# Optimization experiments

Measured on AMD Instinct MI355X. Metric: run time of the kernel, lower is better.

Reference implementation:

```python
import jax, jax.numpy as jnp
import numpy as np

B, C, H, W, N = 2, 64, 512, 512, 150000


def setup_inputs() -> dict:
    key = jax.random.key(0)
    k = jax.random.split(key, 6)
    return {
        "before_pseudoimages": jax.random.normal(k[0], (B, C, H, W), jnp.float32),
        "after_pseudoimages": jax.random.normal(k[1], (B, C, H, W), jnp.float32),
        "point_offsets": jax.random.normal(k[2], (B, N, 3), jnp.float32),
        "voxel_coords": jax.random.randint(k[3], (B, N, 3), 0, 512, jnp.int32),
        "W1": jax.random.normal(k[4], (131, 32), jnp.float32) * 0.08,
        "b1": jnp.zeros((32,), jnp.float32),
        "W2": jax.random.normal(k[5], (32, 3), jnp.float32) * 0.18,
        "b2": jnp.zeros((3,), jnp.float32),
    }


def reference(before_pseudoimages, after_pseudoimages, point_offsets, voxel_coords,
              W1, b1, W2, b2):
    # voxel_coords[..., 0] is the Z index, asserted == 0 in the original; unused.
    ys = voxel_coords[..., 1]  # [B, N]
    xs = voxel_coords[..., 2]  # [B, N]

    def gather(img, y, x):
        # img: [C, H, W] -> gathered [N, C]  (matches pseudoimage[:, y, x].T)
        return img[:, y, x].T

    before_vecs = jax.vmap(gather)(before_pseudoimages, ys, xs)  # [B, N, C]
    after_vecs = jax.vmap(gather)(after_pseudoimages, ys, xs)    # [B, N, C]
    feats = jnp.concatenate([before_vecs, after_vecs, point_offsets], axis=-1)  # [B, N, 131]

    h = jax.nn.gelu(jnp.einsum("bnf,fh->bnh", feats, W1) + b1, approximate=False)
    flow = jnp.einsum("bnh,ho->bno", h, W2) + b2  # [B, N, 3]
    return flow
```

## Files before the change

### kernel.cpp

```cpp
#include <hip/hip_runtime.h>
#include <math.h>

#define NCH   64
#define IMW   512
#define NPTS  150000
#define TOTAL (2 * NPTS)
#define IMHW  (512 * 512)
#define HID   32
#define NBINS 32768


__global__ __launch_bounds__(256) void hist_kernel(const int* __restrict__ coords,
                                                   int* __restrict__ hist) {
    int gid = blockIdx.x * blockDim.x + threadIdx.x;
    if (gid >= TOTAL) return;
    const int y = coords[gid * 3 + 1];
    const int x = coords[gid * 3 + 2];
    const int b = (gid >= NPTS) ? 1 : 0;
    const int key = (b << 14) | (y << 5) | (x >> 4);
    atomicAdd(&hist[key], 1);
}

__global__ __launch_bounds__(1024) void scan_kernel(const int* __restrict__ hist,
                                                    int* __restrict__ binPos) {
    __shared__ int lds[1024];
    const int t = threadIdx.x;
    const int base = t * 32;
    int loc[32];
    int s = 0;
    #pragma unroll
    for (int i = 0; i < 32; ++i) { loc[i] = s; s += hist[base + i]; }
    lds[t] = s;
    __syncthreads();
    for (int d = 1; d < 1024; d <<= 1) {
        int v = lds[t];
        int add = (t >= d) ? lds[t - d] : 0;
        __syncthreads();
        lds[t] = v + add;
        __syncthreads();
    }
    const int excl = lds[t] - s;
    #pragma unroll
    for (int i = 0; i < 32; ++i) binPos[base + i] = excl + loc[i];
}

__global__ __launch_bounds__(256) void scatter_kernel(const int* __restrict__ coords,
                                                      int* __restrict__ binPos,
                                                      int* __restrict__ perm) {
    int gid = blockIdx.x * blockDim.x + threadIdx.x;
    if (gid >= TOTAL) return;
    const int y = coords[gid * 3 + 1];
    const int x = coords[gid * 3 + 2];
    const int b = (gid >= NPTS) ? 1 : 0;
    const int key = (b << 14) | (y << 5) | (x >> 4);
    const int pos = atomicAdd(&binPos[key], 1);
    perm[pos] = gid;
}


#define LOADCH(buf, cbase)                                             \
    _Pragma("unroll")                                                  \
    for (int j = 0; j < 16; ++j) buf[j] = img_ptr[(long)((cbase) + j) * IMHW];

#define FMACH(buf, cbase)                                              \
    _Pragma("unroll")                                                  \
    for (int j = 0; j < 16; ++j) {                                     \
        const float* wr = w1b + ((cbase) + j) * HID;                   \
        _Pragma("unroll")                                              \
        for (int h = 0; h < HID; ++h) acc[h] = fmaf(buf[j], wr[h], acc[h]); \
    }

__global__ __launch_bounds__(256) void ffd_kernel(
    const float* __restrict__ before,
    const float* __restrict__ after,
    const float* __restrict__ offsets,
    const int*   __restrict__ coords,
    const float* __restrict__ W1,
    const float* __restrict__ b1,
    const float* __restrict__ W2,
    const float* __restrict__ b2,
    const int*   __restrict__ perm,
    float*       __restrict__ out)
{
    __shared__ float xch[HID][128];

    const int lp  = threadIdx.x & 127;
    const int img = __builtin_amdgcn_readfirstlane(threadIdx.x >> 7);
    const int gpt = blockIdx.x * 128 + lp;
    const bool valid = gpt < TOTAL;

    int pid = 0;
    if (valid) pid = perm ? perm[gpt] : gpt;

    const long pbase = (long)pid * 3;
    int y = 0, x = 0;
    if (valid) { y = coords[pbase + 1]; x = coords[pbase + 2]; }
    const int b = (pid >= NPTS) ? 1 : 0;

    const float* img_ptr = (img ? after : before) +
                           (long)b * NCH * IMHW + (long)y * IMW + x;
    const float* w1b = W1 + img * 64 * HID;

    float acc[HID];
    if (img == 0) {
        float o0 = 0.f, o1 = 0.f, o2 = 0.f;
        if (valid) { o0 = offsets[pbase]; o1 = offsets[pbase + 1]; o2 = offsets[pbase + 2]; }
        const float* r0 = W1 + 128 * HID;
        const float* r1 = W1 + 129 * HID;
        const float* r2 = W1 + 130 * HID;
        #pragma unroll
        for (int h = 0; h < HID; ++h)
            acc[h] = fmaf(o2, r2[h], fmaf(o1, r1[h], fmaf(o0, r0[h], b1[h])));
    } else {
        #pragma unroll
        for (int h = 0; h < HID; ++h) acc[h] = 0.f;
    }

    if (valid) {
        float g0[16], g1[16];
        LOADCH(g0, 0)
        LOADCH(g1, 16)
        FMACH(g0, 0)
        LOADCH(g0, 32)
        FMACH(g1, 16)
        LOADCH(g1, 48)
        FMACH(g0, 32)
        FMACH(g1, 48)
    }

    if (img == 1) {
        #pragma unroll
        for (int h = 0; h < HID; ++h) xch[h][lp] = acc[h];
    }
    __syncthreads();
    if (img == 0 && valid) {
        #pragma unroll
        for (int h = 0; h < HID; ++h) acc[h] += xch[h][lp];

        #pragma unroll
        for (int h = 0; h < HID; ++h) {
            const float xh = acc[h];
            acc[h] = 0.5f * xh * (1.0f + erff(xh * 0.70710678118654752f));
        }

        float o0 = b2[0], o1 = b2[1], o2 = b2[2];
        #pragma unroll
        for (int h = 0; h < HID; ++h) {
            o0 = fmaf(acc[h], W2[h * 3 + 0], o0);
            o1 = fmaf(acc[h], W2[h * 3 + 1], o1);
            o2 = fmaf(acc[h], W2[h * 3 + 2], o2);
        }
        out[pbase + 0] = o0;
        out[pbase + 1] = o1;
        out[pbase + 2] = o2;
    }
}

extern "C" void kernel_launch(void* const* d_in, const int* in_sizes, int n_in,
                              void* d_out, int out_size, void* d_ws, size_t ws_size,
                              hipStream_t stream) {
    const float* before  = (const float*)d_in[0];
    const float* after   = (const float*)d_in[1];
    const float* offsets = (const float*)d_in[2];
    const int*   coords  = (const int*)  d_in[3];
    const float* W1      = (const float*)d_in[4];
    const float* b1      = (const float*)d_in[5];
    const float* W2      = (const float*)d_in[6];
    const float* b2      = (const float*)d_in[7];
    float* out = (float*)d_out;

    const int block = 256;
    const int sgrid = (TOTAL + block - 1) / block;
    const int fgrid = (TOTAL + 127) / 128;

    const size_t need = (size_t)(2 * NBINS + TOTAL) * sizeof(int);

    if (ws_size >= need) {
        int* hist   = (int*)d_ws;
        int* binPos = hist + NBINS;
        int* perm   = binPos + NBINS;

        hipMemsetAsync(hist, 0, NBINS * sizeof(int), stream);
        hist_kernel<<<sgrid, block, 0, stream>>>(coords, hist);
        scan_kernel<<<1, 1024, 0, stream>>>(hist, binPos);
        scatter_kernel<<<sgrid, block, 0, stream>>>(coords, binPos, perm);
        ffd_kernel<<<fgrid, block, 0, stream>>>(before, after, offsets, coords,
                                                W1, b1, W2, b2, perm, out);
    } else {
        ffd_kernel<<<fgrid, block, 0, stream>>>(before, after, offsets, coords,
                                                W1, b1, W2, b2, nullptr, out);
    }
}
```

Baseline: 119.3 us.

## Split channel reduction across four waves per point, loading all 32 channels upfront

Each block now handles 64 points with four wavefronts, and each wave reduces 32 channels of one image half instead of two waves each doing 64 channels. Partial hidden sums from three waves are combined through shared memory by wave 0, which then applies GELU and the output layer. Each wave issues all 32 gather loads before any FMA, to expose more memory-level parallelism. The cost is twice as many blocks, duplicated index loads, a larger LDS reduction, and higher register pressure from the 32-element load buffer.

```diff
diff --git a/kernel.cpp b/kernel.cpp
--- a/kernel.cpp
+++ b/kernel.cpp
@@ -58,18 +58,6 @@
 }
 
 
-#define LOADCH(buf, cbase)                                             \
-    _Pragma("unroll")                                                  \
-    for (int j = 0; j < 16; ++j) buf[j] = img_ptr[(long)((cbase) + j) * IMHW];
-
-#define FMACH(buf, cbase)                                              \
-    _Pragma("unroll")                                                  \
-    for (int j = 0; j < 16; ++j) {                                     \
-        const float* wr = w1b + ((cbase) + j) * HID;                   \
-        _Pragma("unroll")                                              \
-        for (int h = 0; h < HID; ++h) acc[h] = fmaf(buf[j], wr[h], acc[h]); \
-    }
-
 __global__ __launch_bounds__(256) void ffd_kernel(
     const float* __restrict__ before,
     const float* __restrict__ after,
@@ -82,29 +70,36 @@
     const int*   __restrict__ perm,
     float*       __restrict__ out)
 {
-    __shared__ float xch[HID][128];
+    __shared__ float xch[3][HID][64];
 
-    const int lp  = threadIdx.x & 127;
-    const int img = __builtin_amdgcn_readfirstlane(threadIdx.x >> 7);
-    const int gpt = blockIdx.x * 128 + lp;
+    const int lane = threadIdx.x & 63;
+    const int w    = __builtin_amdgcn_readfirstlane(threadIdx.x >> 6);
+    int gpt = blockIdx.x * 64 + lane;
     const bool valid = gpt < TOTAL;
+    if (!valid) gpt = TOTAL - 1;
 
-    int pid = 0;
-    if (valid) pid = perm ? perm[gpt] : gpt;
+    const int pid = perm ? perm[gpt] : gpt;
+    const long pbase = (long)pid * 3;
 
-    const long pbase = (long)pid * 3;
-    int y = 0, x = 0;
-    if (valid) { y = coords[pbase + 1]; x = coords[pbase + 2]; }
+    const int y = coords[pbase + 1];
+    const int x = coords[pbase + 2];
     const int b = (pid >= NPTS) ? 1 : 0;
 
-    const float* img_ptr = (img ? after : before) +
-                           (long)b * NCH * IMHW + (long)y * IMW + x;
-    const float* w1b = W1 + img * 64 * HID;
+    const float* ibase  = (w < 2) ? before : after;
+    const float* img_ptr = ibase + (long)b * NCH * IMHW
+                         + (long)(w & 1) * 32 * IMHW
+                         + (long)y * IMW + x;
+    const float* w1b = W1 + w * 32 * HID;
+
+    float g[32];
+    #pragma unroll
+    for (int j = 0; j < 32; ++j) g[j] = img_ptr[(long)j * IMHW];
 
     float acc[HID];
-    if (img == 0) {
-        float o0 = 0.f, o1 = 0.f, o2 = 0.f;
-        if (valid) { o0 = offsets[pbase]; o1 = offsets[pbase + 1]; o2 = offsets[pbase + 2]; }
+    if (w == 0) {
+        const float o0 = offsets[pbase];
+        const float o1 = offsets[pbase + 1];
+        const float o2 = offsets[pbase + 2];
         const float* r0 = W1 + 128 * HID;
         const float* r1 = W1 + 129 * HID;
         const float* r2 = W1 + 130 * HID;
@@ -116,26 +111,23 @@
         for (int h = 0; h < HID; ++h) acc[h] = 0.f;
     }
 
-    if (valid) {
-        float g0[16], g1[16];
-        LOADCH(g0, 0)
-        LOADCH(g1, 16)
-        FMACH(g0, 0)
-        LOADCH(g0, 32)
-        FMACH(g1, 16)
-        LOADCH(g1, 48)
-        FMACH(g0, 32)
-        FMACH(g1, 48)
+    #pragma unroll
+    for (int j = 0; j < 32; ++j) {
+        const float* wr = w1b + j * HID;
+        #pragma unroll
+        for (int h = 0; h < HID; ++h) acc[h] = fmaf(g[j], wr[h], acc[h]);
     }
 
-    if (img == 1) {
+    if (w > 0) {
         #pragma unroll
-        for (int h = 0; h < HID; ++h) xch[h][lp] = acc[h];
+        for (int h = 0; h < HID; ++h) xch[w - 1][h][lane] = acc[h];
     }
     __syncthreads();
-    if (img == 0 && valid) {
+
+    if (w == 0 && valid) {
         #pragma unroll
-        for (int h = 0; h < HID; ++h) acc[h] += xch[h][lp];
+        for (int h = 0; h < HID; ++h)
+            acc[h] += xch[0][h][lane] + xch[1][h][lane] + xch[2][h][lane];
 
         #pragma unroll
         for (int h = 0; h < HID; ++h) {
@@ -171,7 +163,7 @@
 
     const int block = 256;
     const int sgrid = (TOTAL + block - 1) / block;
-    const int fgrid = (TOTAL + 127) / 128;
+    const int fgrid = (TOTAL + 63) / 64;
 
     const size_t need = (size_t)(2 * NBINS + TOTAL) * sizeof(int);
 
```

New measurement: 125.9 us. 5.5% more time.
